# Kernel tuning notes

Hardware: AMD Instinct MI355X
Metric: run time of the kernel (lower is better)

The kernel has to match this reference:

```python
import jax, jax.numpy as jnp
import numpy as np

N, M, D = 131072, 128, 128

def setup_inputs() -> dict:
    key = jax.random.key(0)
    k1, k2, k3 = jax.random.split(key, 3)
    X = jax.random.normal(k1, (N, D), dtype=jnp.float32)
    r = jax.random.uniform(k2, (N, M), dtype=jnp.float32)
    mus = jax.random.normal(k3, (M, D), dtype=jnp.float32)
    return {"X": X, "r": r, "mus": mus}

def reference(X, r, mus):
    # Squared pairwise L2 distances without materializing [N, M, D]:
    x2 = jnp.sum(X * X, axis=1)            # [N]
    mu2 = jnp.sum(mus * mus, axis=1)       # [M]
    cross = X @ mus.T                      # [N, M]
    dist2 = jnp.maximum(x2[:, None] + mu2[None, :] - 2.0 * cross, 0.0)
    loss = jnp.sum(r * dist2) / X.shape[0]
    return loss
```

## Files before the change

kernel.cpp:

```cpp
#include <hip/hip_runtime.h>
#include <hip/hip_bf16.h>


typedef __attribute__((ext_vector_type(8)))  short  short8;
typedef __attribute__((ext_vector_type(16))) float  float16v;

#define LDSP 136

#if defined(__has_builtin)
#if __has_builtin(__builtin_amdgcn_cvt_pk_bf16_f32)
#define HAVE_PK_BF16 1
#endif
#endif

__device__ __forceinline__ unsigned int pk_bf16(float x, float y) {
#ifdef HAVE_PK_BF16
    typedef __attribute__((ext_vector_type(2))) __bf16 bf16x2;
    bf16x2 p = __builtin_amdgcn_cvt_pk_bf16_f32(x, y);
    return __builtin_bit_cast(unsigned int, p);
#else
    unsigned int ux = __float_as_uint(x);
    unsigned int uy = __float_as_uint(y);
    ux += 0x7fffu + ((ux >> 16) & 1u);
    uy += 0x7fffu + ((uy >> 16) & 1u);
    return (ux >> 16) | (uy & 0xffff0000u);
#endif
}

__global__ void zero_ws_kernel(float* ws) { ws[threadIdx.x] = 0.0f; }

__global__ void final_reduce_kernel(const float* ws, float* out) {
    const int lane = threadIdx.x;
    float t = ws[lane];
    #pragma unroll
    for (int off = 32; off > 0; off >>= 1) t += __shfl_down(t, off);
    if (lane == 0) out[0] = t * (1.0f / 131072.0f);
}

__global__ __launch_bounds__(256, 3)
void isoloss_kernel(const float* __restrict__ X,
                    const float* __restrict__ r,
                    const float* __restrict__ mus,
                    float* __restrict__ ws)
{
    const int tid  = threadIdx.x;
    const int blk  = blockIdx.x;
    const int wave = tid >> 6;
    const int lane = tid & 63;
    const int col  = lane & 31;
    const int half = lane >> 5;

    __shared__ unsigned short ldsA[128 * LDSP];
    __shared__ float x2s[128];
    __shared__ float wsum[4];

    const float* xbase = X + (size_t)blk * 128 * 128;
    float4 xv[16];
    #pragma unroll
    for (int it = 0; it < 16; ++it)
        xv[it] = *(const float4*)(xbase + (size_t)(it * 256 + tid) * 4);

    #pragma unroll
    for (int it = 0; it < 16; ++it) {
        const float4 v = xv[it];
        float p = v.x*v.x + v.y*v.y + v.z*v.z + v.w*v.w;
        p += __shfl_xor(p, 16);
        p += __shfl_xor(p, 8);
        p += __shfl_xor(p, 4);
        p += __shfl_xor(p, 2);
        p += __shfl_xor(p, 1);
        const int row = it * 8 + (tid >> 5);
        if ((tid & 31) == 0) x2s[row] = p;
        uint2 h;
        h.x = pk_bf16(v.x, v.y);
        h.y = pk_bf16(v.z, v.w);
        *(uint2*)&ldsA[row * LDSP + (tid & 31) * 4] = h;
    }

    short8 bfrag[8];
    float mu2p = 0.0f;
    {
        const float* mrow = mus + (size_t)(wave * 32 + col) * 128 + half * 8;
        #pragma unroll
        for (int ks = 0; ks < 8; ++ks) {
            const float4 a = *(const float4*)(mrow + ks * 16);
            const float4 b = *(const float4*)(mrow + ks * 16 + 4);
            mu2p += a.x*a.x + a.y*a.y + a.z*a.z + a.w*a.w
                  + b.x*b.x + b.y*b.y + b.z*b.z + b.w*b.w;
            union { short8 s8; uint4 u4; } u;
            u.u4.x = pk_bf16(a.x, a.y);
            u.u4.y = pk_bf16(a.z, a.w);
            u.u4.z = pk_bf16(b.x, b.y);
            u.u4.w = pk_bf16(b.z, b.w);
            bfrag[ks] = u.s8;
        }
    }
    const float mu2 = mu2p + __shfl_xor(mu2p, 32);

    __syncthreads();

    float s = 0.0f;
    #pragma unroll
    for (int mt = 0; mt < 4; ++mt) {
        const float* rp = r + (size_t)(blk * 128 + mt * 32) * 128 + wave * 32 + col;
        float rv[16];
        #pragma unroll
        for (int reg = 0; reg < 16; ++reg) {
            const int rl = (reg & 3) + 8 * (reg >> 2) + 4 * half;
            rv[reg] = rp[(size_t)rl * 128];
        }

        float16v acc = {};
        #pragma unroll
        for (int ks = 0; ks < 8; ++ks) {
            const short8 af = *(const short8*)&ldsA[(mt * 32 + col) * LDSP + ks * 16 + half * 8];
            acc = __builtin_amdgcn_mfma_f32_32x32x16_bf16(af, bfrag[ks], acc, 0, 0, 0);
        }

        float4 xq[4];
        #pragma unroll
        for (int q = 0; q < 4; ++q)
            xq[q] = *(const float4*)&x2s[mt * 32 + q * 8 + half * 4];

        #pragma unroll
        for (int reg = 0; reg < 16; ++reg) {
            const float d = fmaxf(xq[reg >> 2][reg & 3] + mu2 - 2.0f * acc[reg], 0.0f);
            s += rv[reg] * d;
        }
    }

    #pragma unroll
    for (int off = 32; off > 0; off >>= 1) s += __shfl_down(s, off);
    if (lane == 0) wsum[wave] = s;
    __syncthreads();
    if (tid == 0)
        atomicAdd(&ws[blk & 63], wsum[0] + wsum[1] + wsum[2] + wsum[3]);
}

extern "C" void kernel_launch(void* const* d_in, const int* in_sizes, int n_in,
                              void* d_out, int out_size, void* d_ws, size_t ws_size,
                              hipStream_t stream) {
    const float* X   = (const float*)d_in[0];
    const float* r   = (const float*)d_in[1];
    const float* mus = (const float*)d_in[2];
    float* out = (float*)d_out;
    float* ws  = (float*)d_ws;

    zero_ws_kernel<<<1, 64, 0, stream>>>(ws);
    isoloss_kernel<<<1024, 256, 0, stream>>>(X, r, mus, ws);
    final_reduce_kernel<<<1, 64, 0, stream>>>(ws, out);
}
```

Measured before the change: 149.6 us.

## Software-pipeline X and r loads across 32-row M sub-tiles

```diff
diff --git a/kernel.cpp b/kernel.cpp
--- a/kernel.cpp
+++ b/kernel.cpp
@@ -55,26 +55,18 @@
     __shared__ float wsum[4];
 
     const float* xbase = X + (size_t)blk * 128 * 128;
-    float4 xv[16];
+    const float* rbase = r + (size_t)blk * 128 * 128 + wave * 32 + col;
+
+    float4 xv[4];
     #pragma unroll
-    for (int it = 0; it < 16; ++it)
+    for (int it = 0; it < 4; ++it)
         xv[it] = *(const float4*)(xbase + (size_t)(it * 256 + tid) * 4);
 
+    float rv[2][16];
     #pragma unroll
-    for (int it = 0; it < 16; ++it) {
-        const float4 v = xv[it];
-        float p = v.x*v.x + v.y*v.y + v.z*v.z + v.w*v.w;
-        p += __shfl_xor(p, 16);
-        p += __shfl_xor(p, 8);
-        p += __shfl_xor(p, 4);
-        p += __shfl_xor(p, 2);
-        p += __shfl_xor(p, 1);
-        const int row = it * 8 + (tid >> 5);
-        if ((tid & 31) == 0) x2s[row] = p;
-        uint2 h;
-        h.x = pk_bf16(v.x, v.y);
-        h.y = pk_bf16(v.z, v.w);
-        *(uint2*)&ldsA[row * LDSP + (tid & 31) * 4] = h;
+    for (int reg = 0; reg < 16; ++reg) {
+        const int rl = (reg & 3) + 8 * (reg >> 2) + 4 * half;
+        rv[0][reg] = rbase[(size_t)rl * 128];
     }
 
     short8 bfrag[8];
@@ -97,17 +89,41 @@
     }
     const float mu2 = mu2p + __shfl_xor(mu2p, 32);
 
+    #pragma unroll
+    for (int it = 0; it < 4; ++it) {
+        const float4 v = xv[it];
+        float p = v.x*v.x + v.y*v.y + v.z*v.z + v.w*v.w;
+        p += __shfl_xor(p, 16);
+        p += __shfl_xor(p, 8);
+        p += __shfl_xor(p, 4);
+        p += __shfl_xor(p, 2);
+        p += __shfl_xor(p, 1);
+        const int row = it * 8 + (tid >> 5);
+        if ((tid & 31) == 0) x2s[row] = p;
+        uint2 h;
+        h.x = pk_bf16(v.x, v.y);
+        h.y = pk_bf16(v.z, v.w);
+        *(uint2*)&ldsA[row * LDSP + (tid & 31) * 4] = h;
+    }
+
     __syncthreads();
 
     float s = 0.0f;
     #pragma unroll
     for (int mt = 0; mt < 4; ++mt) {
-        const float* rp = r + (size_t)(blk * 128 + mt * 32) * 128 + wave * 32 + col;
-        float rv[16];
-        #pragma unroll
-        for (int reg = 0; reg < 16; ++reg) {
-            const int rl = (reg & 3) + 8 * (reg >> 2) + 4 * half;
-            rv[reg] = rp[(size_t)rl * 128];
+        const int cur = mt & 1;
+        const int nxt = cur ^ 1;
+
+        float4 xn[4];
+        if (mt < 3) {
+            #pragma unroll
+            for (int it = 0; it < 4; ++it)
+                xn[it] = *(const float4*)(xbase + (size_t)((mt + 1) * 1024 + it * 256 + tid) * 4);
+            #pragma unroll
+            for (int reg = 0; reg < 16; ++reg) {
+                const int rl = (reg & 3) + 8 * (reg >> 2) + 4 * half;
+                rv[nxt][reg] = rbase[(size_t)((mt + 1) * 32 + rl) * 128];
+            }
         }
 
         float16v acc = {};
@@ -121,11 +137,30 @@
         #pragma unroll
         for (int q = 0; q < 4; ++q)
             xq[q] = *(const float4*)&x2s[mt * 32 + q * 8 + half * 4];
-
         #pragma unroll
         for (int reg = 0; reg < 16; ++reg) {
             const float d = fmaxf(xq[reg >> 2][reg & 3] + mu2 - 2.0f * acc[reg], 0.0f);
-            s += rv[reg] * d;
+            s += rv[cur][reg] * d;
+        }
+
+        if (mt < 3) {
+            #pragma unroll
+            for (int it = 0; it < 4; ++it) {
+                const float4 v = xn[it];
+                float p = v.x*v.x + v.y*v.y + v.z*v.z + v.w*v.w;
+                p += __shfl_xor(p, 16);
+                p += __shfl_xor(p, 8);
+                p += __shfl_xor(p, 4);
+                p += __shfl_xor(p, 2);
+                p += __shfl_xor(p, 1);
+                const int row = (mt + 1) * 32 + it * 8 + (tid >> 5);
+                if ((tid & 31) == 0) x2s[row] = p;
+                uint2 h;
+                h.x = pk_bf16(v.x, v.y);
+                h.y = pk_bf16(v.z, v.w);
+                *(uint2*)&ldsA[row * LDSP + (tid & 31) * 4] = h;
+            }
+            __syncthreads();
         }
     }
 
```

After: 233.2 us. 1.56x slower.

## Reformulate loss as r·mus projection then dot with X, drop max clamp

Applied to the files above, without the earlier changes.

```diff
diff --git a/kernel.cpp b/kernel.cpp
--- a/kernel.cpp
+++ b/kernel.cpp
@@ -4,8 +4,6 @@
 
 typedef __attribute__((ext_vector_type(8)))  short  short8;
 typedef __attribute__((ext_vector_type(16))) float  float16v;
-
-#define LDSP 136
 
 #if defined(__has_builtin)
 #if __has_builtin(__builtin_amdgcn_cvt_pk_bf16_f32)
@@ -27,8 +25,6 @@
 #endif
 }
 
-__global__ void zero_ws_kernel(float* ws) { ws[threadIdx.x] = 0.0f; }
-
 __global__ void final_reduce_kernel(const float* ws, float* out) {
     const int lane = threadIdx.x;
     float t = ws[lane];
@@ -37,104 +33,119 @@
     if (lane == 0) out[0] = t * (1.0f / 131072.0f);
 }
 
-__global__ __launch_bounds__(256, 3)
+__global__ __launch_bounds__(256)
+void build_afrag_kernel(const float* __restrict__ mus, uint4* __restrict__ afrag,
+                        float* __restrict__ ws)
+{
+    const int g = blockIdx.x * 256 + threadIdx.x;
+    if (blockIdx.x == 0 && threadIdx.x < 64) ws[threadIdx.x] = 0.0f;
+
+    const int dt   = g >> 9;
+    const int rem  = g & 511;
+    const int ks   = rem >> 6;
+    const int lane = rem & 63;
+    const int dp   = dt * 32 + (lane & 31);
+    const int m0   = ks * 16 + (lane >> 5) * 8;
+
+    float v[8];
+    if (dp < 128) {
+        #pragma unroll
+        for (int e = 0; e < 8; ++e)
+            v[e] = mus[(size_t)(m0 + e) * 128 + dp];
+    } else if (dp == 128) {
+        #pragma unroll
+        for (int e = 0; e < 8; ++e) {
+            const float4* row = (const float4*)(mus + (size_t)(m0 + e) * 128);
+            float a = 0.0f;
+            #pragma unroll 8
+            for (int d4 = 0; d4 < 32; ++d4) {
+                const float4 t = row[d4];
+                a += t.x*t.x + t.y*t.y + t.z*t.z + t.w*t.w;
+            }
+            v[e] = a;
+        }
+    } else if (dp == 129) {
+        #pragma unroll
+        for (int e = 0; e < 8; ++e) v[e] = 1.0f;
+    } else {
+        #pragma unroll
+        for (int e = 0; e < 8; ++e) v[e] = 0.0f;
+    }
+
+    uint4 u;
+    u.x = pk_bf16(v[0], v[1]);
+    u.y = pk_bf16(v[2], v[3]);
+    u.z = pk_bf16(v[4], v[5]);
+    u.w = pk_bf16(v[6], v[7]);
+    afrag[g] = u;
+}
+
+__global__ __launch_bounds__(256, 4)
 void isoloss_kernel(const float* __restrict__ X,
                     const float* __restrict__ r,
-                    const float* __restrict__ mus,
+                    const uint4* __restrict__ afrag,
                     float* __restrict__ ws)
 {
     const int tid  = threadIdx.x;
-    const int blk  = blockIdx.x;
-    const int wave = tid >> 6;
+    const int w    = blockIdx.x * 4 + (tid >> 6);
     const int lane = tid & 63;
     const int col  = lane & 31;
     const int half = lane >> 5;
 
-    __shared__ unsigned short ldsA[128 * LDSP];
-    __shared__ float x2s[128];
-    __shared__ float wsum[4];
+    const size_t i = (size_t)w * 32 + col;
+    const float* rrow_p = r + i * 128;
+    const float* xrow_p = X + i * 128;
 
-    const float* xbase = X + (size_t)blk * 128 * 128;
-    float4 xv[16];
+    short8 bfrag[8];
     #pragma unroll
-    for (int it = 0; it < 16; ++it)
-        xv[it] = *(const float4*)(xbase + (size_t)(it * 256 + tid) * 4);
+    for (int ks = 0; ks < 8; ++ks) {
+        const float4 a = *(const float4*)(rrow_p + ks * 16 + half * 8);
+        const float4 b = *(const float4*)(rrow_p + ks * 16 + half * 8 + 4);
+        union { short8 s8; uint4 u4; } u;
+        u.u4.x = pk_bf16(a.x, a.y);
+        u.u4.y = pk_bf16(a.z, a.w);
+        u.u4.z = pk_bf16(b.x, b.y);
+        u.u4.w = pk_bf16(b.z, b.w);
+        bfrag[ks] = u.s8;
+    }
+
+    float dotp = 0.0f, x2p = 0.0f, rmu2v = 0.0f, rrowv = 0.0f;
 
     #pragma unroll
-    for (int it = 0; it < 16; ++it) {
-        const float4 v = xv[it];
-        float p = v.x*v.x + v.y*v.y + v.z*v.z + v.w*v.w;
-        p += __shfl_xor(p, 16);
-        p += __shfl_xor(p, 8);
-        p += __shfl_xor(p, 4);
-        p += __shfl_xor(p, 2);
-        p += __shfl_xor(p, 1);
-        const int row = it * 8 + (tid >> 5);
-        if ((tid & 31) == 0) x2s[row] = p;
-        uint2 h;
-        h.x = pk_bf16(v.x, v.y);
-        h.y = pk_bf16(v.z, v.w);
-        *(uint2*)&ldsA[row * LDSP + (tid & 31) * 4] = h;
-    }
-
-    short8 bfrag[8];
-    float mu2p = 0.0f;
-    {
-        const float* mrow = mus + (size_t)(wave * 32 + col) * 128 + half * 8;
+    for (int dt = 0; dt < 5; ++dt) {
+        short8 af[8];
         #pragma unroll
-        for (int ks = 0; ks < 8; ++ks) {
-            const float4 a = *(const float4*)(mrow + ks * 16);
-            const float4 b = *(const float4*)(mrow + ks * 16 + 4);
-            mu2p += a.x*a.x + a.y*a.y + a.z*a.z + a.w*a.w
-                  + b.x*b.x + b.y*b.y + b.z*b.z + b.w*b.w;
-            union { short8 s8; uint4 u4; } u;
-            u.u4.x = pk_bf16(a.x, a.y);
-            u.u4.y = pk_bf16(a.z, a.w);
-            u.u4.z = pk_bf16(b.x, b.y);
-            u.u4.w = pk_bf16(b.z, b.w);
-            bfrag[ks] = u.s8;
-        }
-    }
-    const float mu2 = mu2p + __shfl_xor(mu2p, 32);
-
-    __syncthreads();
-
-    float s = 0.0f;
-    #pragma unroll
-    for (int mt = 0; mt < 4; ++mt) {
-        const float* rp = r + (size_t)(blk * 128 + mt * 32) * 128 + wave * 32 + col;
-        float rv[16];
-        #pragma unroll
-        for (int reg = 0; reg < 16; ++reg) {
-            const int rl = (reg & 3) + 8 * (reg >> 2) + 4 * half;
-            rv[reg] = rp[(size_t)rl * 128];
-        }
+        for (int ks = 0; ks < 8; ++ks)
+            af[ks] = ((const short8*)afrag)[(dt * 8 + ks) * 64 + lane];
 
         float16v acc = {};
         #pragma unroll
-        for (int ks = 0; ks < 8; ++ks) {
-            const short8 af = *(const short8*)&ldsA[(mt * 32 + col) * LDSP + ks * 16 + half * 8];
-            acc = __builtin_amdgcn_mfma_f32_32x32x16_bf16(af, bfrag[ks], acc, 0, 0, 0);
-        }
+        for (int ks = 0; ks < 8; ++ks)
+            acc = __builtin_amdgcn_mfma_f32_32x32x16_bf16(af[ks], bfrag[ks], acc, 0, 0, 0);
 
-        float4 xq[4];
-        #pragma unroll
-        for (int q = 0; q < 4; ++q)
-            xq[q] = *(const float4*)&x2s[mt * 32 + q * 8 + half * 4];
-
-        #pragma unroll
-        for (int reg = 0; reg < 16; ++reg) {
-            const float d = fmaxf(xq[reg >> 2][reg & 3] + mu2 - 2.0f * acc[reg], 0.0f);
-            s += rv[reg] * d;
+        if (dt < 4) {
+            float4 xq[4];
+            #pragma unroll
+            for (int q = 0; q < 4; ++q)
+                xq[q] = *(const float4*)(xrow_p + dt * 32 + q * 8 + half * 4);
+            #pragma unroll
+            for (int reg = 0; reg < 16; ++reg) {
+                const float x = xq[reg >> 2][reg & 3];
+                dotp += x * acc[reg];
+                x2p  += x * x;
+            }
+        } else {
+            rmu2v = acc[0];
+            rrowv = acc[1];
         }
     }
 
+    const float x2i = x2p + __shfl_xor(x2p, 32);
+    float s = x2i * rrowv + rmu2v - 2.0f * dotp;
+
     #pragma unroll
     for (int off = 32; off > 0; off >>= 1) s += __shfl_down(s, off);
-    if (lane == 0) wsum[wave] = s;
-    __syncthreads();
-    if (tid == 0)
-        atomicAdd(&ws[blk & 63], wsum[0] + wsum[1] + wsum[2] + wsum[3]);
+    if (lane == 0) atomicAdd(&ws[blockIdx.x & 63], s);
 }
 
 extern "C" void kernel_launch(void* const* d_in, const int* in_sizes, int n_in,
@@ -145,8 +156,9 @@
     const float* mus = (const float*)d_in[2];
     float* out = (float*)d_out;
     float* ws  = (float*)d_ws;
+    uint4* afrag = (uint4*)((char*)d_ws + 256);
 
-    zero_ws_kernel<<<1, 64, 0, stream>>>(ws);
-    isoloss_kernel<<<1024, 256, 0, stream>>>(X, r, mus, ws);
+    build_afrag_kernel<<<10, 256, 0, stream>>>(mus, afrag, ws);
+    isoloss_kernel<<<1024, 256, 0, stream>>>(X, r, afrag, ws);
     final_reduce_kernel<<<1, 64, 0, stream>>>(ws, out);
 }
```

Result: slower. 183.3 us (+22.6%).
